# Optimization experiments

Hardware: AMD Instinct MI355X
Metric: run time of the kernel (lower is better)

Reference implementation:

```python
import jax, jax.numpy as jnp
import numpy as np

N_INP = 1024
N_HID = 1024
N_OUT = 1024
B, S = 8, 2048


def setup_inputs() -> dict:
    key = jax.random.key(0)
    ks = jax.random.split(key, 9)
    s_in = 1.0 / np.sqrt(N_INP)
    s_hid = 1.0 / np.sqrt(N_HID)
    return {
        "x": jax.random.normal(ks[0], (B, S, N_INP), jnp.float32),
        "wq": jax.random.uniform(ks[1], (N_INP, N_HID), jnp.float32, -s_in, s_in),
        "bq": jax.random.uniform(ks[2], (N_HID,), jnp.float32, -s_in, s_in),
        "wk": jax.random.uniform(ks[3], (N_INP, N_HID), jnp.float32, -s_in, s_in),
        "bk": jax.random.uniform(ks[4], (N_HID,), jnp.float32, -s_in, s_in),
        "wv": jax.random.uniform(ks[5], (N_INP, N_HID), jnp.float32, -s_in, s_in),
        "bv": jax.random.uniform(ks[6], (N_HID,), jnp.float32, -s_in, s_in),
        "wo": jax.random.uniform(ks[7], (N_HID, N_OUT), jnp.float32, -s_hid, s_hid),
        "bo": jax.random.uniform(ks[8], (N_OUT,), jnp.float32, -s_hid, s_hid),
    }


def reference(x, wq, bq, wk, bk, wv, bv, wo, bo):
    # x: [B, S, n_inp]
    q = jnp.einsum("bsi,ih->bsh", x, wq) + bq  # [B,S,H]
    k = jnp.einsum("bsi,ih->bsh", x, wk) + bk
    v = jnp.einsum("bsi,ih->bsh", x, wv) + bv
    scale = 1.0 / jnp.sqrt(jnp.float32(N_HID))
    energy = jnp.einsum("bqh,bkh->bqk", q, k) * scale  # [B,S,S]
    attn = jax.nn.softmax(energy, axis=-1)  # dropout=0.0 (eval)
    ctx = jnp.einsum("bqk,bkh->bqh", attn, v)  # [B,S,H]
    out = jnp.einsum("bsh,ho->bso", ctx, wo) + bo  # [B,S,n_out]
    return out
```

## Files before the change

### kernel.cpp

```cpp
#include <hip/hip_runtime.h>
#include <hip/hip_bf16.h>


typedef __attribute__((ext_vector_type(8))) __bf16 bf16x8;
typedef __attribute__((ext_vector_type(4))) __bf16 bf16x4;
typedef __attribute__((ext_vector_type(4))) float  f32x4;
typedef __attribute__((ext_vector_type(8))) float  f32x8;

__device__ __forceinline__ void gl_lds16(const void* g, void* l) {
    __builtin_amdgcn_global_load_lds(
        (__attribute__((address_space(1))) const void*)g,
        (__attribute__((address_space(3))) void*)l, 16, 0, 0);
}

template <bool SWP>
__device__ __forceinline__ f32x4 mfma16(bf16x8 a, bf16x8 b, f32x4 c) {
    if constexpr (SWP)
        return __builtin_amdgcn_mfma_f32_16x16x32_bf16(b, a, c, 0, 0, 0);
    else
        return __builtin_amdgcn_mfma_f32_16x16x32_bf16(a, b, c, 0, 0, 0);
}

__global__ __launch_bounds__(256) void k_convert(const float* __restrict__ in,
                                                 __bf16* __restrict__ out) {
    const int i = blockIdx.x * 256 + threadIdx.x;
    f32x8 a = *((const f32x8*)in + i);
    bf16x8 o;
#pragma unroll
    for (int j = 0; j < 8; ++j) o[j] = (__bf16)a[j];
    *((bf16x8*)out + i) = o;
}

__global__ __launch_bounds__(256) void k_transpose_w(
    const float* __restrict__ w0, const float* __restrict__ w1,
    const float* __restrict__ w2, const float* __restrict__ w3,
    __bf16* __restrict__ Wt) {
    const int z = blockIdx.z;
    const float* W = (z == 0) ? w0 : (z == 1) ? w1 : (z == 2) ? w2 : w3;
    __bf16* Wo = Wt + (long long)z * 1048576;
    __shared__ float t[64][65];
    const int tid = threadIdx.x;
    const int c4 = (tid & 15) * 4, r0 = tid >> 4;
    const int bx = blockIdx.x * 64, by = blockIdx.y * 64;
#pragma unroll
    for (int p = 0; p < 4; ++p) {
        const int r = r0 + p * 16;
        f32x4 v = *(const f32x4*)(W + (long long)(by + r) * 1024 + bx + c4);
#pragma unroll
        for (int j = 0; j < 4; ++j) t[r][c4 + j] = v[j];
    }
    __syncthreads();
#pragma unroll
    for (int p = 0; p < 4; ++p) {
        const int r = r0 + p * 16;
        bf16x4 o;
#pragma unroll
        for (int j = 0; j < 4; ++j) o[j] = (__bf16)t[c4 + j][r];
        *(bf16x4*)(Wo + (long long)(bx + r) * 1024 + by + c4) = o;
    }
}

__global__ __launch_bounds__(256) void k_bcat(const float* __restrict__ bq,
                                              const float* __restrict__ bk,
                                              const float* __restrict__ bv,
                                              float* __restrict__ bc) {
    const int i = blockIdx.x * 256 + threadIdx.x;
    const float* s = (i < 1024) ? bq : (i < 2048 ? bk : bv);
    bc[i] = s[i & 1023];
}

__global__ __launch_bounds__(256) void k_softmax(__bf16* __restrict__ E) {
    __bf16* p = E + (long long)blockIdx.x * 2048;
    const int tid = threadIdx.x, l = tid & 63, w = tid >> 6;
    bf16x8 vb = *((const bf16x8*)p + tid);
    float v[8];
#pragma unroll
    for (int i = 0; i < 8; ++i) v[i] = (float)vb[i];
    float m = v[0];
#pragma unroll
    for (int i = 1; i < 8; ++i) m = fmaxf(m, v[i]);
    for (int off = 32; off > 0; off >>= 1) m = fmaxf(m, __shfl_xor(m, off));
    __shared__ float redm[4], reds[4];
    if (l == 0) redm[w] = m;
    __syncthreads();
    m = fmaxf(fmaxf(redm[0], redm[1]), fmaxf(redm[2], redm[3]));
    float e[8], s = 0.f;
#pragma unroll
    for (int i = 0; i < 8; ++i) { e[i] = __expf(v[i] - m); s += e[i]; }
    for (int off = 32; off > 0; off >>= 1) s += __shfl_xor(s, off);
    if (l == 0) reds[w] = s;
    __syncthreads();
    s = reds[0] + reds[1] + reds[2] + reds[3];
    const float inv = 1.0f / s;
    bf16x8 o;
#pragma unroll
    for (int i = 0; i < 8; ++i) o[i] = (__bf16)(e[i] * inv);
    *((bf16x8*)p + tid) = o;
}

template <int MODE, bool HAS_BIAS>
__global__ __launch_bounds__(512, 2) void gemm_bt(
    const __bf16* __restrict__ A, const __bf16* __restrict__ Bt,
    const float* __restrict__ bias, void* __restrict__ Cout,
    int K, int lda, int ldb, int ldc, int gy, int rpx, int bnc,
    float scale, long long sA, long long sB, long long sC) {
    constexpr bool SWP = (MODE != 4);
    __shared__ __align__(16) __bf16 Abuf0[16384];
    __shared__ __align__(16) __bf16 Bbuf0[16384];
    __shared__ __align__(16) __bf16 Abuf1[16384];
    __shared__ __align__(16) __bf16 Bbuf1[16384];

    const int lid = blockIdx.x;
    const int xcd = lid & 7;
    const int jj = lid >> 3;
    const int bn = jj % bnc;
    const int rt = xcd * rpx + jj / bnc;
    const int z = rt / gy;
    const int bm = rt - z * gy;

    const __bf16* Ab = A + (long long)z * sA;
    const __bf16* Bb = Bt + (long long)z * sB;

    const int tid = threadIdx.x;
    const int l = tid & 63, w = tid >> 6;
    const int wm = w >> 2, wn = w & 3;

    const int rA = tid >> 3;
    const int cswz = (tid & 7) ^ (rA & 7);
    const __bf16* aSg = Ab + (long long)(bm * 256 + rA) * lda + cswz * 8;
    const __bf16* bSg = Bb + (long long)(bn * 256 + rA) * ldb + cswz * 8;
    const long long a64 = (long long)lda * 64;
    const long long b64 = (long long)ldb * 64;
    const int ldst = tid * 16;

    const int r16 = l & 15, kq4 = l >> 4;
    const int sw0 = kq4 ^ (r16 & 7);
    const int aro0 = (wm * 128 + r16) * 64 + sw0 * 8;
    const int aro1 = aro0 ^ 32;
    const int bro0 = (wn * 64 + r16) * 64 + sw0 * 8;
    const int bro1 = bro0 ^ 32;

    f32x4 acc[8][4] = {};
    bf16x8 bf[4][2];

#define ST_A(buf, j, t)                                                    \
    gl_lds16(aSg + (j) * a64 + (long long)(t) * 64,                        \
             (char*)(buf) + ldst + (j) * 8192)
#define ST_B(buf, j, t)                                                    \
    gl_lds16(bSg + (j) * b64 + (long long)(t) * 64,                        \
             (char*)(buf) + ldst + (j) * 8192)

#define RD_B(buf)                                                          \
    do {                                                                   \
        _Pragma("unroll") for (int ni = 0; ni < 4; ++ni) {                 \
            bf[ni][0] = *(const bf16x8*)((buf) + bro0 + ni * 1024);        \
            bf[ni][1] = *(const bf16x8*)((buf) + bro1 + ni * 1024);        \
        }                                                                  \
    } while (0)

#define WV4 asm volatile("s_waitcnt vmcnt(4)" ::: "memory")
#define WV0 asm volatile("s_waitcnt vmcnt(0)" ::: "memory")
#define NOW ((void)0)

#define PHASE(Abuf, p, RB, RBUF, STAGES, WAIT)                                 \
    do {                                                                      \
        bf16x8 af0k0 = *(const bf16x8*)((Abuf) + aro0 + (2 * (p)) * 1024);     \
        bf16x8 af0k1 = *(const bf16x8*)((Abuf) + aro1 + (2 * (p)) * 1024);     \
        bf16x8 af1k0 = *(const bf16x8*)((Abuf) + aro0 + (2 * (p) + 1) * 1024); \
        bf16x8 af1k1 = *(const bf16x8*)((Abuf) + aro1 + (2 * (p) + 1) * 1024); \
        if (RB) RD_B(RBUF);                                                   \
        STAGES;                                                               \
        __builtin_amdgcn_s_barrier();                                         \
        asm volatile("s_waitcnt lgkmcnt(0)" ::: "memory");                    \
        __builtin_amdgcn_sched_barrier(0);                                    \
        __builtin_amdgcn_s_setprio(1);                                        \
        _Pragma("unroll") for (int ni = 0; ni < 4; ++ni) {                    \
            acc[2 * (p)][ni] = mfma16<SWP>(af0k0, bf[ni][0], acc[2*(p)][ni]); \
            acc[2 * (p)][ni] = mfma16<SWP>(af0k1, bf[ni][1], acc[2*(p)][ni]); \
            acc[2*(p)+1][ni] = mfma16<SWP>(af1k0, bf[ni][0], acc[2*(p)+1][ni]);\
            acc[2*(p)+1][ni] = mfma16<SWP>(af1k1, bf[ni][1], acc[2*(p)+1][ni]);\
        }                                                                     \
        __builtin_amdgcn_s_setprio(0);                                        \
        WAIT;                                                                 \
        __builtin_amdgcn_sched_barrier(0);                                    \
        __builtin_amdgcn_s_barrier();                                         \
    } while (0)

    ST_B(Bbuf0, 0, 0); ST_B(Bbuf0, 1, 0); ST_B(Bbuf0, 2, 0); ST_B(Bbuf0, 3, 0);
    ST_A(Abuf0, 0, 0); ST_A(Abuf0, 1, 0); ST_A(Abuf0, 2, 0); ST_A(Abuf0, 3, 0);
    ST_B(Bbuf1, 0, 1); ST_B(Bbuf1, 1, 1); ST_B(Bbuf1, 2, 1); ST_B(Bbuf1, 3, 1);
    WV4;
    __builtin_amdgcn_s_barrier();

    const int NT = K >> 6;
    for (int t0 = 0; t0 + 3 < NT; t0 += 2) {
        PHASE(Abuf0, 0, 1, Bbuf0,
              (ST_A(Abuf1, 0, t0 + 1), ST_A(Abuf1, 1, t0 + 1),
               ST_A(Abuf1, 2, t0 + 1), ST_A(Abuf1, 3, t0 + 1)), NOW);
        PHASE(Abuf0, 1, 0, Bbuf0,
              (ST_B(Bbuf0, 0, t0 + 2), ST_B(Bbuf0, 1, t0 + 2)), NOW);
        PHASE(Abuf0, 2, 0, Bbuf0,
              (ST_B(Bbuf0, 2, t0 + 2), ST_B(Bbuf0, 3, t0 + 2)), NOW);
        PHASE(Abuf0, 3, 0, Bbuf0, NOW, WV4);
        PHASE(Abuf1, 0, 1, Bbuf1,
              (ST_A(Abuf0, 0, t0 + 2), ST_A(Abuf0, 1, t0 + 2)), NOW);
        PHASE(Abuf1, 1, 0, Bbuf1,
              (ST_A(Abuf0, 2, t0 + 2), ST_A(Abuf0, 3, t0 + 2)), NOW);
        PHASE(Abuf1, 2, 0, Bbuf1,
              (ST_B(Bbuf1, 0, t0 + 3), ST_B(Bbuf1, 1, t0 + 3)), NOW);
        PHASE(Abuf1, 3, 0, Bbuf1,
              (ST_B(Bbuf1, 2, t0 + 3), ST_B(Bbuf1, 3, t0 + 3)), WV4);
    }
    {
        PHASE(Abuf0, 0, 1, Bbuf0,
              (ST_A(Abuf1, 0, NT - 1), ST_A(Abuf1, 1, NT - 1),
               ST_A(Abuf1, 2, NT - 1), ST_A(Abuf1, 3, NT - 1)), NOW);
        PHASE(Abuf0, 1, 0, Bbuf0, NOW, NOW);
        PHASE(Abuf0, 2, 0, Bbuf0, NOW, NOW);
        PHASE(Abuf0, 3, 0, Bbuf0, NOW, WV0);
        PHASE(Abuf1, 0, 1, Bbuf1, NOW, NOW);
        PHASE(Abuf1, 1, 0, Bbuf1, NOW, NOW);
        PHASE(Abuf1, 2, 0, Bbuf1, NOW, NOW);
        PHASE(Abuf1, 3, 0, Bbuf1, NOW, NOW);
    }
#undef ST_A
#undef ST_B
#undef RD_B
#undef WV4
#undef WV0
#undef NOW
#undef PHASE

    const int quad = kq4;
    if constexpr (MODE == 2) {
        __bf16* Qb = (__bf16*)Cout;
        const int part = bn >> 2;
#pragma unroll
        for (int mi = 0; mi < 8; ++mi) {
            const int srow0 = bm * 256 + wm * 128 + mi * 16 + r16;
            const int b = srow0 >> 11;
            const int s0 = srow0 & 2047;
#pragma unroll
            for (int ni = 0; ni < 4; ++ni) {
                const int col0 = bn * 256 + wn * 64 + ni * 16 + quad * 4;
                const f32x4 bb = *(const f32x4*)(bias + col0);
                const int c1 = col0 - part * 1024;
                bf16x4 o;
#pragma unroll
                for (int rr = 0; rr < 4; ++rr) o[rr] = (__bf16)(acc[mi][ni][rr] + bb[rr]);
                *(bf16x4*)(Qb + (long long)part * 16777216 +
                           (long long)b * 2097152 + (long long)s0 * 1024 + c1) = o;
            }
        }
    } else if constexpr (MODE == 4) {
        __bf16* Vb = (__bf16*)Cout;
#pragma unroll
        for (int mi = 0; mi < 8; ++mi) {
            const int srow0 = bm * 256 + wm * 128 + mi * 16 + quad * 4;
            const int b = srow0 >> 11;
            const int s0 = srow0 & 2047;
#pragma unroll
            for (int ni = 0; ni < 4; ++ni) {
                const int c1 = bn * 256 + wn * 64 + ni * 16 + r16;
                const float bb = HAS_BIAS ? bias[c1] : 0.0f;
                bf16x4 o;
#pragma unroll
                for (int rr = 0; rr < 4; ++rr) o[rr] = (__bf16)(acc[mi][ni][rr] + bb);
                *(bf16x4*)(Vb + (long long)b * 2097152 +
                           (long long)c1 * 2048 + s0) = o;
            }
        }
    } else {
        const long long cbase = (long long)z * sC;
#pragma unroll
        for (int mi = 0; mi < 8; ++mi) {
            const int row = bm * 256 + wm * 128 + mi * 16 + r16;
#pragma unroll
            for (int ni = 0; ni < 4; ++ni) {
                const int col0 = bn * 256 + wn * 64 + ni * 16 + quad * 4;
                f32x4 v;
                if constexpr (HAS_BIAS) {
                    const f32x4 bb = *(const f32x4*)(bias + col0);
#pragma unroll
                    for (int rr = 0; rr < 4; ++rr) v[rr] = acc[mi][ni][rr] * scale + bb[rr];
                } else {
#pragma unroll
                    for (int rr = 0; rr < 4; ++rr) v[rr] = acc[mi][ni][rr] * scale;
                }
                if constexpr (MODE == 1) {
                    *(f32x4*)((float*)Cout + cbase + (long long)row * ldc + col0) = v;
                } else {
                    bf16x4 o;
#pragma unroll
                    for (int rr = 0; rr < 4; ++rr) o[rr] = (__bf16)v[rr];
                    *(bf16x4*)((__bf16*)Cout + cbase + (long long)row * ldc + col0) = o;
                }
            }
        }
    }
}

extern "C" void kernel_launch(void* const* d_in, const int* in_sizes, int n_in,
                              void* d_out, int out_size, void* d_ws, size_t ws_size,
                              hipStream_t stream) {
    const float* x  = (const float*)d_in[0];
    const float* wq = (const float*)d_in[1];
    const float* bq = (const float*)d_in[2];
    const float* wk = (const float*)d_in[3];
    const float* bk = (const float*)d_in[4];
    const float* wv = (const float*)d_in[5];
    const float* bv = (const float*)d_in[6];
    const float* wo = (const float*)d_in[7];
    const float* bo = (const float*)d_in[8];
    float* out = (float*)d_out;

    __bf16* ws  = (__bf16*)d_ws;
    __bf16* Xb  = ws;
    __bf16* E   = ws;
    __bf16* Q   = ws + 33554432;
    __bf16* Kb  = ws + 50331648;
    __bf16* Vt  = ws + 67108864;
    __bf16* Ctx = ws + 83886080;
    __bf16* WT  = ws + 100663296;
    float*  bc  = (float*)(ws + 104857600);

    k_convert<<<8192, 256, 0, stream>>>(x, Xb);
    k_transpose_w<<<dim3(16, 16, 4), 256, 0, stream>>>(wq, wk, wv, wo, WT);
    k_bcat<<<12, 256, 0, stream>>>(bq, bk, bv, bc);

    gemm_bt<2, true><<<512, 512, 0, stream>>>(
        Xb, WT, bc, Q, 1024, 1024, 1024, 0, 64, 8, 8, 1.0f, 0, 0, 0);

    gemm_bt<4, true><<<256, 512, 0, stream>>>(
        Xb, WT + 2097152, bc + 2048, Vt, 1024, 1024, 1024, 0, 64, 8, 4,
        1.0f, 0, 0, 0);

    gemm_bt<0, false><<<512, 512, 0, stream>>>(
        Q, Kb, nullptr, E, 1024, 1024, 1024, 2048, 8, 8, 8,
        0.03125f, 2097152, 2097152, 4194304);

    k_softmax<<<16384, 256, 0, stream>>>(E);

    gemm_bt<0, false><<<256, 512, 0, stream>>>(
        E, Vt, nullptr, Ctx, 2048, 2048, 2048, 1024, 8, 8, 4,
        1.0f, 4194304, 2097152, 2097152);

    gemm_bt<1, true><<<256, 512, 0, stream>>>(
        Ctx, WT + 3145728, bo, out, 1024, 1024, 1024, 1024, 64, 8, 4,
        1.0f, 0, 0, 0);
}
```

Before: 446.8 us.

## Fuse prep kernels, pack two softmax rows per block, restructure GEMM barriers

Merges the x conversion, weight transpose and bias concat into one k_prep launch, which removes two kernel launches. Softmax now handles two rows per 512-thread block. In the GEMM main loop, global->LDS staging is issued before the LDS fragment reads. Each phase no longer ends with its own barrier; a barrier is kept only at the vmcnt wait points, and B staging is moved later in the schedule. This cuts synchronisation per phase but risks LDS hazards if the remaining barriers do not cover buffer reuse.

```diff
diff --git a/kernel.cpp b/kernel.cpp
--- a/kernel.cpp
+++ b/kernel.cpp
@@ -21,58 +21,58 @@
         return __builtin_amdgcn_mfma_f32_16x16x32_bf16(a, b, c, 0, 0, 0);
 }
 
-__global__ __launch_bounds__(256) void k_convert(const float* __restrict__ in,
-                                                 __bf16* __restrict__ out) {
-    const int i = blockIdx.x * 256 + threadIdx.x;
-    f32x8 a = *((const f32x8*)in + i);
-    bf16x8 o;
-#pragma unroll
-    for (int j = 0; j < 8; ++j) o[j] = (__bf16)a[j];
-    *((bf16x8*)out + i) = o;
-}
-
-__global__ __launch_bounds__(256) void k_transpose_w(
+__global__ __launch_bounds__(256) void k_prep(
+    const float* __restrict__ x,
     const float* __restrict__ w0, const float* __restrict__ w1,
     const float* __restrict__ w2, const float* __restrict__ w3,
-    __bf16* __restrict__ Wt) {
-    const int z = blockIdx.z;
-    const float* W = (z == 0) ? w0 : (z == 1) ? w1 : (z == 2) ? w2 : w3;
-    __bf16* Wo = Wt + (long long)z * 1048576;
-    __shared__ float t[64][65];
+    const float* __restrict__ bq, const float* __restrict__ bk,
+    const float* __restrict__ bv,
+    __bf16* __restrict__ Xb, __bf16* __restrict__ WT, float* __restrict__ bc) {
+    __shared__ float tsh[64][65];
+    const int bid = blockIdx.x, tid = threadIdx.x;
+    if (bid < 8192) {
+        const int i = bid * 256 + tid;
+        f32x8 a = *((const f32x8*)x + i);
+        bf16x8 o;
+#pragma unroll
+        for (int j = 0; j < 8; ++j) o[j] = (__bf16)a[j];
+        *((bf16x8*)Xb + i) = o;
+    } else if (bid < 9216) {
+        const int tt = bid - 8192;
+        const int z = tt >> 8, rem = tt & 255;
+        const int bx = (rem & 15) * 64, by = (rem >> 4) * 64;
+        const float* W = (z == 0) ? w0 : (z == 1) ? w1 : (z == 2) ? w2 : w3;
+        __bf16* Wo = WT + (long long)z * 1048576;
+        const int c4 = (tid & 15) * 4, r0 = tid >> 4;
+#pragma unroll
+        for (int p = 0; p < 4; ++p) {
+            const int r = r0 + p * 16;
+            f32x4 v = *(const f32x4*)(W + (long long)(by + r) * 1024 + bx + c4);
+#pragma unroll
+            for (int j = 0; j < 4; ++j) tsh[r][c4 + j] = v[j];
+        }
+        __syncthreads();
+#pragma unroll
+        for (int p = 0; p < 4; ++p) {
+            const int r = r0 + p * 16;
+            bf16x4 o;
+#pragma unroll
+            for (int j = 0; j < 4; ++j) o[j] = (__bf16)tsh[c4 + j][r];
+            *(bf16x4*)(Wo + (long long)(bx + r) * 1024 + by + c4) = o;
+        }
+    } else {
+        const int i = (bid - 9216) * 256 + tid;
+        const float* s = (i < 1024) ? bq : (i < 2048 ? bk : bv);
+        bc[i] = s[i & 1023];
+    }
+}
+
+__global__ __launch_bounds__(512) void k_softmax(__bf16* __restrict__ E) {
     const int tid = threadIdx.x;
-    const int c4 = (tid & 15) * 4, r0 = tid >> 4;
-    const int bx = blockIdx.x * 64, by = blockIdx.y * 64;
-#pragma unroll
-    for (int p = 0; p < 4; ++p) {
-        const int r = r0 + p * 16;
-        f32x4 v = *(const f32x4*)(W + (long long)(by + r) * 1024 + bx + c4);
-#pragma unroll
-        for (int j = 0; j < 4; ++j) t[r][c4 + j] = v[j];
-    }
-    __syncthreads();
-#pragma unroll
-    for (int p = 0; p < 4; ++p) {
-        const int r = r0 + p * 16;
-        bf16x4 o;
-#pragma unroll
-        for (int j = 0; j < 4; ++j) o[j] = (__bf16)t[c4 + j][r];
-        *(bf16x4*)(Wo + (long long)(bx + r) * 1024 + by + c4) = o;
-    }
-}
-
-__global__ __launch_bounds__(256) void k_bcat(const float* __restrict__ bq,
-                                              const float* __restrict__ bk,
-                                              const float* __restrict__ bv,
-                                              float* __restrict__ bc) {
-    const int i = blockIdx.x * 256 + threadIdx.x;
-    const float* s = (i < 1024) ? bq : (i < 2048 ? bk : bv);
-    bc[i] = s[i & 1023];
-}
-
-__global__ __launch_bounds__(256) void k_softmax(__bf16* __restrict__ E) {
-    __bf16* p = E + (long long)blockIdx.x * 2048;
-    const int tid = threadIdx.x, l = tid & 63, w = tid >> 6;
-    bf16x8 vb = *((const bf16x8*)p + tid);
+    const int half = tid >> 8, t = tid & 255;
+    __bf16* p = E + ((long long)blockIdx.x * 2 + half) * 2048;
+    const int l = tid & 63, w4 = (tid >> 6) & 3;
+    bf16x8 vb = *((const bf16x8*)p + t);
     float v[8];
 #pragma unroll
     for (int i = 0; i < 8; ++i) v[i] = (float)vb[i];
@@ -80,22 +80,23 @@
 #pragma unroll
     for (int i = 1; i < 8; ++i) m = fmaxf(m, v[i]);
     for (int off = 32; off > 0; off >>= 1) m = fmaxf(m, __shfl_xor(m, off));
-    __shared__ float redm[4], reds[4];
-    if (l == 0) redm[w] = m;
+    __shared__ float redm[2][4], reds[2][4];
+    if (l == 0) redm[half][w4] = m;
     __syncthreads();
-    m = fmaxf(fmaxf(redm[0], redm[1]), fmaxf(redm[2], redm[3]));
+    m = fmaxf(fmaxf(redm[half][0], redm[half][1]),
+              fmaxf(redm[half][2], redm[half][3]));
     float e[8], s = 0.f;
 #pragma unroll
     for (int i = 0; i < 8; ++i) { e[i] = __expf(v[i] - m); s += e[i]; }
     for (int off = 32; off > 0; off >>= 1) s += __shfl_xor(s, off);
-    if (l == 0) reds[w] = s;
+    if (l == 0) reds[half][w4] = s;
     __syncthreads();
-    s = reds[0] + reds[1] + reds[2] + reds[3];
+    s = reds[half][0] + reds[half][1] + reds[half][2] + reds[half][3];
     const float inv = 1.0f / s;
     bf16x8 o;
 #pragma unroll
     for (int i = 0; i < 8; ++i) o[i] = (__bf16)(e[i] * inv);
-    *((bf16x8*)p + tid) = o;
+    *((bf16x8*)p + t) = o;
 }
 
 template <int MODE, bool HAS_BIAS>
@@ -158,21 +159,33 @@
         }                                                                  \
     } while (0)
 
+#define BARR                                                               \
+    do {                                                                   \
+        __builtin_amdgcn_sched_barrier(0);                                 \
+        __builtin_amdgcn_s_barrier();                                      \
+        __builtin_amdgcn_sched_barrier(0);                                 \
+    } while (0)
+#define LGK0                                                               \
+    do {                                                                   \
+        asm volatile("s_waitcnt lgkmcnt(0)" ::: "memory");                 \
+        __builtin_amdgcn_sched_barrier(0);                                 \
+    } while (0)
 #define WV4 asm volatile("s_waitcnt vmcnt(4)" ::: "memory")
 #define WV0 asm volatile("s_waitcnt vmcnt(0)" ::: "memory")
 #define NOW ((void)0)
-
-#define PHASE(Abuf, p, RB, RBUF, STAGES, WAIT)                                 \
+#define TS4 do { WV4; BARR; } while (0)
+#define TS0 do { WV0; BARR; } while (0)
+
+#define PHASE(Abuf, p, RB, RBUF, STAGES, TAILOP)                               \
     do {                                                                      \
+        STAGES;                                                               \
         bf16x8 af0k0 = *(const bf16x8*)((Abuf) + aro0 + (2 * (p)) * 1024);     \
         bf16x8 af0k1 = *(const bf16x8*)((Abuf) + aro1 + (2 * (p)) * 1024);     \
         bf16x8 af1k0 = *(const bf16x8*)((Abuf) + aro0 + (2 * (p) + 1) * 1024); \
         bf16x8 af1k1 = *(const bf16x8*)((Abuf) + aro1 + (2 * (p) + 1) * 1024); \
         if (RB) RD_B(RBUF);                                                   \
-        STAGES;                                                               \
-        __builtin_amdgcn_s_barrier();                                         \
-        asm volatile("s_waitcnt lgkmcnt(0)" ::: "memory");                    \
-        __builtin_amdgcn_sched_barrier(0);                                    \
+        BARR;                                                                 \
+        LGK0;                                                                 \
         __builtin_amdgcn_s_setprio(1);                                        \
         _Pragma("unroll") for (int ni = 0; ni < 4; ++ni) {                    \
             acc[2 * (p)][ni] = mfma16<SWP>(af0k0, bf[ni][0], acc[2*(p)][ni]); \
@@ -181,27 +194,25 @@
             acc[2*(p)+1][ni] = mfma16<SWP>(af1k1, bf[ni][1], acc[2*(p)+1][ni]);\
         }                                                                     \
         __builtin_amdgcn_s_setprio(0);                                        \
-        WAIT;                                                                 \
-        __builtin_amdgcn_sched_barrier(0);                                    \
-        __builtin_amdgcn_s_barrier();                                         \
+        TAILOP;                                                               \
     } while (0)
 
     ST_B(Bbuf0, 0, 0); ST_B(Bbuf0, 1, 0); ST_B(Bbuf0, 2, 0); ST_B(Bbuf0, 3, 0);
     ST_A(Abuf0, 0, 0); ST_A(Abuf0, 1, 0); ST_A(Abuf0, 2, 0); ST_A(Abuf0, 3, 0);
     ST_B(Bbuf1, 0, 1); ST_B(Bbuf1, 1, 1); ST_B(Bbuf1, 2, 1); ST_B(Bbuf1, 3, 1);
     WV4;
-    __builtin_amdgcn_s_barrier();
+    BARR;
 
     const int NT = K >> 6;
     for (int t0 = 0; t0 + 3 < NT; t0 += 2) {
         PHASE(Abuf0, 0, 1, Bbuf0,
               (ST_A(Abuf1, 0, t0 + 1), ST_A(Abuf1, 1, t0 + 1),
                ST_A(Abuf1, 2, t0 + 1), ST_A(Abuf1, 3, t0 + 1)), NOW);
-        PHASE(Abuf0, 1, 0, Bbuf0,
+        PHASE(Abuf0, 1, 0, Bbuf0, NOW, NOW);
+        PHASE(Abuf0, 2, 0, Bbuf0,
               (ST_B(Bbuf0, 0, t0 + 2), ST_B(Bbuf0, 1, t0 + 2)), NOW);
-        PHASE(Abuf0, 2, 0, Bbuf0,
-              (ST_B(Bbuf0, 2, t0 + 2), ST_B(Bbuf0, 3, t0 + 2)), NOW);
-        PHASE(Abuf0, 3, 0, Bbuf0, NOW, WV4);
+        PHASE(Abuf0, 3, 0, Bbuf0,
+              (ST_B(Bbuf0, 2, t0 + 2), ST_B(Bbuf0, 3, t0 + 2)), TS4);
         PHASE(Abuf1, 0, 1, Bbuf1,
               (ST_A(Abuf0, 0, t0 + 2), ST_A(Abuf0, 1, t0 + 2)), NOW);
         PHASE(Abuf1, 1, 0, Bbuf1,
@@ -209,7 +220,7 @@
         PHASE(Abuf1, 2, 0, Bbuf1,
               (ST_B(Bbuf1, 0, t0 + 3), ST_B(Bbuf1, 1, t0 + 3)), NOW);
         PHASE(Abuf1, 3, 0, Bbuf1,
-              (ST_B(Bbuf1, 2, t0 + 3), ST_B(Bbuf1, 3, t0 + 3)), WV4);
+              (ST_B(Bbuf1, 2, t0 + 3), ST_B(Bbuf1, 3, t0 + 3)), TS4);
     }
     {
         PHASE(Abuf0, 0, 1, Bbuf0,
@@ -217,7 +228,7 @@
                ST_A(Abuf1, 2, NT - 1), ST_A(Abuf1, 3, NT - 1)), NOW);
         PHASE(Abuf0, 1, 0, Bbuf0, NOW, NOW);
         PHASE(Abuf0, 2, 0, Bbuf0, NOW, NOW);
-        PHASE(Abuf0, 3, 0, Bbuf0, NOW, WV0);
+        PHASE(Abuf0, 3, 0, Bbuf0, NOW, TS0);
         PHASE(Abuf1, 0, 1, Bbuf1, NOW, NOW);
         PHASE(Abuf1, 1, 0, Bbuf1, NOW, NOW);
         PHASE(Abuf1, 2, 0, Bbuf1, NOW, NOW);
@@ -226,9 +237,13 @@
 #undef ST_A
 #undef ST_B
 #undef RD_B
+#undef BARR
+#undef LGK0
 #undef WV4
 #undef WV0
 #undef NOW
+#undef TS4
+#undef TS0
 #undef PHASE
 
     const int quad = kq4;
@@ -324,9 +339,7 @@
     __bf16* WT  = ws + 100663296;
     float*  bc  = (float*)(ws + 104857600);
 
-    k_convert<<<8192, 256, 0, stream>>>(x, Xb);
-    k_transpose_w<<<dim3(16, 16, 4), 256, 0, stream>>>(wq, wk, wv, wo, WT);
-    k_bcat<<<12, 256, 0, stream>>>(bq, bk, bv, bc);
+    k_prep<<<9228, 256, 0, stream>>>(x, wq, wk, wv, wo, bq, bk, bv, Xb, WT, bc);
 
     gemm_bt<2, true><<<512, 512, 0, stream>>>(
         Xb, WT, bc, Q, 1024, 1024, 1024, 0, 64, 8, 8, 1.0f, 0, 0, 0);
@@ -339,7 +352,7 @@
         Q, Kb, nullptr, E, 1024, 1024, 1024, 2048, 8, 8, 8,
         0.03125f, 2097152, 2097152, 4194304);
 
-    k_softmax<<<16384, 256, 0, stream>>>(E);
+    k_softmax<<<8192, 512, 0, stream>>>(E);
 
     gemm_bt<0, false><<<256, 512, 0, stream>>>(
         E, Vt, nullptr, Ctx, 2048, 2048, 2048, 1024, 8, 8, 4,
```

Result: faster. 431.2 us (-3.5%).
